# Kernel optimization log

Measured on AMD Instinct MI355X. Metric: run time of the kernel, lower is better.

The kernel has to match this reference:

```python
import jax, jax.numpy as jnp
import numpy as np

EPS = 1e-7  # K.epsilon()

def setup_inputs() -> dict:
    key = jax.random.key(0)
    k1, k2, k3 = jax.random.split(key, 3)
    B, T, D = 32, 2048, 512
    x = jax.random.normal(k1, (B, T, D), dtype=jnp.float32)
    W = jax.random.normal(k2, (D, D), dtype=jnp.float32) * (1.0 / np.sqrt(D))
    b = jnp.zeros((D,), dtype=jnp.float32)
    u = jax.random.normal(k3, (D,), dtype=jnp.float32) * (1.0 / np.sqrt(D))
    return {"x": x, "W": W, "b": b, "u": u}

def reference(x, W, b, u):
    # uit = tanh(x @ W + b)  -> [B, T, D]
    uit = jnp.tanh(jnp.einsum('btd,de->bte', x, W) + b)
    # scores: sum over feature dim of uit * u -> [B, T]
    ait = jnp.einsum('btd,d->bt', uit, u)
    # exp + normalize over T (no mask); matches original exp/sum form
    a = jnp.exp(ait)
    a = a / (jnp.sum(a, axis=1, keepdims=True) + EPS)
    # weighted sum pooling over T -> [B, D]
    return jnp.einsum('btd,bt->bd', x, a)
```

## Files before the change

kernel.cpp:

```cpp
#include <hip/hip_runtime.h>
#include <math.h>

#define D_DIM 512

typedef short short8v __attribute__((ext_vector_type(8)));
typedef unsigned short ushort8v __attribute__((ext_vector_type(8)));
typedef float f32x16 __attribute__((ext_vector_type(16)));

__device__ inline unsigned short f2bf(float f) {
    union { float f; unsigned int u; } a; a.f = f;
    unsigned int u = a.u;
    unsigned int r = (u + 0x7fffu + ((u >> 16) & 1u)) >> 16;
    return (unsigned short)r;
}

__global__ __launch_bounds__(256) void wt_kernel(const float* __restrict__ W,
                                                 unsigned short* __restrict__ Wb) {
    int g = blockIdx.x * 256 + threadIdx.x;
    int k = g >> 7;
    int e4 = (g & 127) * 4;
    float4 v = *(const float4*)(W + (size_t)k * D_DIM + e4);
    Wb[(size_t)(e4 + 0) * D_DIM + k] = f2bf(v.x);
    Wb[(size_t)(e4 + 1) * D_DIM + k] = f2bf(v.y);
    Wb[(size_t)(e4 + 2) * D_DIM + k] = f2bf(v.z);
    Wb[(size_t)(e4 + 3) * D_DIM + k] = f2bf(v.w);
}

constexpr int LDE = 40;

__global__ __launch_bounds__(256, 2) void gemm_ait_mfma(
    const float* __restrict__ x, const unsigned short* __restrict__ Wb,
    const float* __restrict__ bias, const float* __restrict__ u,
    float* __restrict__ ait)
{
    __shared__ __align__(16) unsigned short xs[64 * LDE];
    __shared__ __align__(16) unsigned short wsh[512 * LDE];
    __shared__ float rowpart[4][64];

    const int tid  = threadIdx.x;
    const int wave = tid >> 6;
    const int lane = tid & 63;
    const int half = lane >> 5;
    const int nl   = lane & 31;
    const int m0   = blockIdx.x * 64;

    f32x16 acc[2][4];
    #pragma unroll
    for (int mi = 0; mi < 2; ++mi)
        #pragma unroll
        for (int ni = 0; ni < 4; ++ni)
            #pragma unroll
            for (int r = 0; r < 16; ++r) acc[mi][ni][r] = 0.f;

    const int xr = tid >> 2;
    const int xc = tid & 3;

    for (int kk = 0; kk < D_DIM; kk += 32) {
        {
            const float* xp = x + (size_t)(m0 + xr) * D_DIM + kk + xc * 8;
            float4 a0 = *(const float4*)xp;
            float4 a1 = *(const float4*)(xp + 4);
            ushort8v pk;
            pk[0] = f2bf(a0.x); pk[1] = f2bf(a0.y); pk[2] = f2bf(a0.z); pk[3] = f2bf(a0.w);
            pk[4] = f2bf(a1.x); pk[5] = f2bf(a1.y); pk[6] = f2bf(a1.z); pk[7] = f2bf(a1.w);
            *(ushort8v*)&xs[xr * LDE + xc * 8] = pk;
        }
        #pragma unroll
        for (int p = 0; p < 8; ++p) {
            int chunk = tid + p * 256;
            int e  = chunk >> 2;
            int ci = chunk & 3;
            ushort8v wv = *(const ushort8v*)&Wb[(size_t)e * D_DIM + kk + ci * 8];
            *(ushort8v*)&wsh[e * LDE + ci * 8] = wv;
        }
        __syncthreads();

        #pragma unroll
        for (int ks = 0; ks < 2; ++ks) {
            short8v af[2], bfr[4];
            #pragma unroll
            for (int mi = 0; mi < 2; ++mi)
                af[mi] = *(const short8v*)&xs[(mi * 32 + nl) * LDE + ks * 16 + half * 8];
            #pragma unroll
            for (int ni = 0; ni < 4; ++ni)
                bfr[ni] = *(const short8v*)&wsh[(wave * 128 + ni * 32 + nl) * LDE + ks * 16 + half * 8];
            #pragma unroll
            for (int mi = 0; mi < 2; ++mi)
                #pragma unroll
                for (int ni = 0; ni < 4; ++ni)
                    acc[mi][ni] = __builtin_amdgcn_mfma_f32_32x32x16_bf16(
                        af[mi], bfr[ni], acc[mi][ni], 0, 0, 0);
        }
        __syncthreads();
    }

    float rowsum[2][16];
    #pragma unroll
    for (int mi = 0; mi < 2; ++mi)
        #pragma unroll
        for (int r = 0; r < 16; ++r) rowsum[mi][r] = 0.f;

    #pragma unroll
    for (int mi = 0; mi < 2; ++mi) {
        #pragma unroll
        for (int ni = 0; ni < 4; ++ni) {
            int col = wave * 128 + ni * 32 + nl;
            float be = bias[col], ue = u[col];
            #pragma unroll
            for (int r = 0; r < 16; ++r)
                rowsum[mi][r] += tanhf(acc[mi][ni][r] + be) * ue;
        }
    }
    #pragma unroll
    for (int mi = 0; mi < 2; ++mi)
        #pragma unroll
        for (int r = 0; r < 16; ++r) {
            float v = rowsum[mi][r];
            v += __shfl_xor(v, 1, 64);
            v += __shfl_xor(v, 2, 64);
            v += __shfl_xor(v, 4, 64);
            v += __shfl_xor(v, 8, 64);
            v += __shfl_xor(v, 16, 64);
            rowsum[mi][r] = v;
        }
    if (nl == 0) {
        #pragma unroll
        for (int mi = 0; mi < 2; ++mi)
            #pragma unroll
            for (int r = 0; r < 16; ++r) {
                int row = mi * 32 + (r & 3) + 8 * (r >> 2) + 4 * half;
                rowpart[wave][row] = rowsum[mi][r];
            }
    }
    __syncthreads();
    if (tid < 64)
        ait[m0 + tid] = rowpart[0][tid] + rowpart[1][tid] + rowpart[2][tid] + rowpart[3][tid];
}

__global__ __launch_bounds__(256) void gemm_ait_f32(
    const float* __restrict__ x, const float* __restrict__ W,
    const float* __restrict__ bias, const float* __restrict__ u,
    float* __restrict__ ait)
{
    __shared__ float xsf[64][68];
    __shared__ float wshf[64][132];
    const int tid = threadIdx.x;
    const int tx = tid & 15, ty = tid >> 4;
    const int m0 = blockIdx.x * 64;
    float rowsum[4] = {0.f, 0.f, 0.f, 0.f};
    for (int e0 = 0; e0 < D_DIM; e0 += 128) {
        float acc[4][8];
        #pragma unroll
        for (int i = 0; i < 4; ++i)
            #pragma unroll
            for (int j = 0; j < 8; ++j) acc[i][j] = 0.f;
        for (int kc = 0; kc < D_DIM; kc += 64) {
            #pragma unroll
            for (int i = 0; i < 4; ++i) {
                int idx = tid + i * 256;
                int r = idx >> 4, c = (idx & 15) * 4;
                *(float4*)&xsf[r][c] = *(const float4*)(x + (size_t)(m0 + r) * D_DIM + kc + c);
            }
            #pragma unroll
            for (int i = 0; i < 8; ++i) {
                int idx = tid + i * 256;
                int r = idx >> 5, c = (idx & 31) * 4;
                *(float4*)&wshf[r][c] = *(const float4*)(W + (size_t)(kc + r) * D_DIM + e0 + c);
            }
            __syncthreads();
            #pragma unroll 4
            for (int k = 0; k < 64; ++k) {
                float xv[4];
                #pragma unroll
                for (int i = 0; i < 4; ++i) xv[i] = xsf[ty * 4 + i][k];
                float4 w0 = *(const float4*)&wshf[k][tx * 8];
                float4 w1 = *(const float4*)&wshf[k][tx * 8 + 4];
                #pragma unroll
                for (int i = 0; i < 4; ++i) {
                    acc[i][0] += xv[i] * w0.x; acc[i][1] += xv[i] * w0.y;
                    acc[i][2] += xv[i] * w0.z; acc[i][3] += xv[i] * w0.w;
                    acc[i][4] += xv[i] * w1.x; acc[i][5] += xv[i] * w1.y;
                    acc[i][6] += xv[i] * w1.z; acc[i][7] += xv[i] * w1.w;
                }
            }
            __syncthreads();
        }
        #pragma unroll
        for (int j = 0; j < 8; ++j) {
            int e = e0 + tx * 8 + j;
            float be = bias[e], ue = u[e];
            #pragma unroll
            for (int i = 0; i < 4; ++i) rowsum[i] += tanhf(acc[i][j] + be) * ue;
        }
    }
    float* red = &xsf[0][0];
    #pragma unroll
    for (int i = 0; i < 4; ++i) red[(ty * 4 + i) * 16 + tx] = rowsum[i];
    __syncthreads();
    if (tid < 64) {
        float s = 0.f;
        #pragma unroll
        for (int j = 0; j < 16; ++j) s += red[tid * 16 + j];
        ait[m0 + tid] = s;
    }
}

__global__ __launch_bounds__(256) void softmax_kernel(float* __restrict__ ait, int T)
{
    const int b = blockIdx.x;
    float* p = ait + (size_t)b * T;
    const int tid = threadIdx.x;
    float ev[8];
    float local = 0.f;
    #pragma unroll
    for (int i = 0; i < 8; ++i) {
        ev[i] = expf(p[tid + i * 256]);
        local += ev[i];
    }
    #pragma unroll
    for (int off = 32; off > 0; off >>= 1)
        local += __shfl_down(local, off, 64);
    __shared__ float wsum[4];
    const int wv = tid >> 6, lane = tid & 63;
    if (lane == 0) wsum[wv] = local;
    __syncthreads();
    float total = wsum[0] + wsum[1] + wsum[2] + wsum[3];
    float inv = 1.0f / (total + 1e-7f);
    #pragma unroll
    for (int i = 0; i < 8; ++i) p[tid + i * 256] = ev[i] * inv;
}

__global__ __launch_bounds__(256) void pool_partial_kernel(
    const float* __restrict__ x, const float* __restrict__ a,
    float* __restrict__ partial, int T)
{
    const int chunks = T >> 8;
    const int b = blockIdx.x / chunks;
    const int c = blockIdx.x % chunks;
    const int tid = threadIdx.x;
    const int th = tid >> 7;
    const int d = (tid & 127) * 4;
    const int t0 = c * 256 + th * 128;

    const float* xp = x + ((size_t)b * T + t0) * D_DIM + d;
    const float* ap = a + (size_t)b * T + t0;

    float4 acc = {0.f, 0.f, 0.f, 0.f};
    for (int t = 0; t < 128; ++t) {
        float s = ap[t];
        float4 xv = *(const float4*)(xp + (size_t)t * D_DIM);
        acc.x += xv.x * s; acc.y += xv.y * s;
        acc.z += xv.z * s; acc.w += xv.w * s;
    }
    __shared__ float4 tmp[128];
    if (th == 1) tmp[tid & 127] = acc;
    __syncthreads();
    if (th == 0) {
        float4 o = tmp[tid];
        acc.x += o.x; acc.y += o.y; acc.z += o.z; acc.w += o.w;
        *(float4*)(partial + (size_t)blockIdx.x * D_DIM + d) = acc;
    }
}

__global__ __launch_bounds__(256) void pool_reduce_kernel(
    const float* __restrict__ partial, float* __restrict__ out, int chunks)
{
    const int b = blockIdx.x;
    const int tid = threadIdx.x;
    const int d = tid * 2;
    float2 acc = {0.f, 0.f};
    for (int c = 0; c < chunks; ++c) {
        float2 v = *(const float2*)(partial + ((size_t)b * chunks + c) * D_DIM + d);
        acc.x += v.x; acc.y += v.y;
    }
    *(float2*)(out + (size_t)b * D_DIM + d) = acc;
}

__global__ __launch_bounds__(256) void pool_atomic_kernel(
    const float* __restrict__ x, const float* __restrict__ a,
    float* __restrict__ out, int T)
{
    const int chunks = T >> 8;
    const int b = blockIdx.x / chunks;
    const int c = blockIdx.x % chunks;
    const int tid = threadIdx.x;
    const int d = tid * 2;
    const int t0 = c * 256;
    const float* xp = x + ((size_t)b * T + t0) * D_DIM + d;
    const float* ap = a + (size_t)b * T + t0;
    float2 acc = {0.f, 0.f};
    for (int t = 0; t < 256; ++t) {
        float s = ap[t];
        float2 xv = *(const float2*)(xp + (size_t)t * D_DIM);
        acc.x += xv.x * s; acc.y += xv.y * s;
    }
    float* o = out + (size_t)b * D_DIM + d;
    atomicAdd(o + 0, acc.x);
    atomicAdd(o + 1, acc.y);
}

extern "C" void kernel_launch(void* const* d_in, const int* in_sizes, int n_in,
                              void* d_out, int out_size, void* d_ws, size_t ws_size,
                              hipStream_t stream)
{
    const float* x    = (const float*)d_in[0];
    const float* W    = (const float*)d_in[1];
    const float* bias = (const float*)d_in[2];
    const float* u    = (const float*)d_in[3];
    float* out = (float*)d_out;

    const int Dd = in_sizes[2];
    const int M  = in_sizes[0] / Dd;
    const int B  = out_size / Dd;
    const int T  = M / B;
    const int chunks = T >> 8;

    const size_t wb_bytes   = (size_t)Dd * Dd * sizeof(unsigned short);
    const size_t ait_bytes  = (size_t)M * sizeof(float);
    const size_t part_bytes = (size_t)B * chunks * Dd * sizeof(float);

    if (ws_size >= wb_bytes + ait_bytes) {
        unsigned short* Wb = (unsigned short*)d_ws;
        float* ait = (float*)((char*)d_ws + wb_bytes);
        wt_kernel<<<dim3((Dd * Dd / 4) / 256), dim3(256), 0, stream>>>(W, Wb);
        gemm_ait_mfma<<<dim3(M / 64), dim3(256), 0, stream>>>(x, Wb, bias, u, ait);
        softmax_kernel<<<dim3(B), dim3(256), 0, stream>>>(ait, T);
        if (ws_size >= wb_bytes + ait_bytes + part_bytes) {
            float* partial = (float*)((char*)d_ws + wb_bytes + ait_bytes);
            pool_partial_kernel<<<dim3(B * chunks), dim3(256), 0, stream>>>(x, ait, partial, T);
            pool_reduce_kernel<<<dim3(B), dim3(256), 0, stream>>>(partial, out, chunks);
        } else {
            hipMemsetAsync(d_out, 0, (size_t)out_size * sizeof(float), stream);
            pool_atomic_kernel<<<dim3(B * chunks), dim3(256), 0, stream>>>(x, ait, out, T);
        }
    } else {
        float* ait = (float*)d_ws;
        gemm_ait_f32<<<dim3(M / 64), dim3(256), 0, stream>>>(x, W, bias, u, ait);
        softmax_kernel<<<dim3(B), dim3(256), 0, stream>>>(ait, T);
        hipMemsetAsync(d_out, 0, (size_t)out_size * sizeof(float), stream);
        pool_atomic_kernel<<<dim3(B * chunks), dim3(256), 0, stream>>>(x, ait, out, T);
    }
}
```

Measured before the change: 288.1 us.

## Prefetch next GEMM tile into registers, use fast tanh, split pooling finer

```diff
diff --git a/kernel.cpp b/kernel.cpp
--- a/kernel.cpp
+++ b/kernel.cpp
@@ -12,6 +12,11 @@
     unsigned int u = a.u;
     unsigned int r = (u + 0x7fffu + ((u >> 16) & 1u)) >> 16;
     return (unsigned short)r;
+}
+
+__device__ inline float fast_tanh(float y) {
+    float e2 = __expf(2.f * y);
+    return 1.f - __fdividef(2.f, e2 + 1.f);
 }
 
 __global__ __launch_bounds__(256) void wt_kernel(const float* __restrict__ W,
@@ -54,26 +59,44 @@
 
     const int xr = tid >> 2;
     const int xc = tid & 3;
+    const float* xbase = x + (size_t)(m0 + xr) * D_DIM + xc * 8;
+
+    int wg_off[8], wl_off[8];
+    #pragma unroll
+    for (int p = 0; p < 8; ++p) {
+        int chunk = tid + p * 256;
+        int e  = chunk >> 2;
+        int ci = chunk & 3;
+        wg_off[p] = e * D_DIM + ci * 8;
+        wl_off[p] = e * LDE + ci * 8;
+    }
+
+    float4 px0 = *(const float4*)(xbase);
+    float4 px1 = *(const float4*)(xbase + 4);
+    ushort8v pw[8];
+    #pragma unroll
+    for (int p = 0; p < 8; ++p)
+        pw[p] = *(const ushort8v*)&Wb[wg_off[p]];
 
     for (int kk = 0; kk < D_DIM; kk += 32) {
         {
-            const float* xp = x + (size_t)(m0 + xr) * D_DIM + kk + xc * 8;
-            float4 a0 = *(const float4*)xp;
-            float4 a1 = *(const float4*)(xp + 4);
             ushort8v pk;
-            pk[0] = f2bf(a0.x); pk[1] = f2bf(a0.y); pk[2] = f2bf(a0.z); pk[3] = f2bf(a0.w);
-            pk[4] = f2bf(a1.x); pk[5] = f2bf(a1.y); pk[6] = f2bf(a1.z); pk[7] = f2bf(a1.w);
+            pk[0] = f2bf(px0.x); pk[1] = f2bf(px0.y); pk[2] = f2bf(px0.z); pk[3] = f2bf(px0.w);
+            pk[4] = f2bf(px1.x); pk[5] = f2bf(px1.y); pk[6] = f2bf(px1.z); pk[7] = f2bf(px1.w);
             *(ushort8v*)&xs[xr * LDE + xc * 8] = pk;
         }
         #pragma unroll
-        for (int p = 0; p < 8; ++p) {
-            int chunk = tid + p * 256;
-            int e  = chunk >> 2;
-            int ci = chunk & 3;
-            ushort8v wv = *(const ushort8v*)&Wb[(size_t)e * D_DIM + kk + ci * 8];
-            *(ushort8v*)&wsh[e * LDE + ci * 8] = wv;
-        }
+        for (int p = 0; p < 8; ++p)
+            *(ushort8v*)&wsh[wl_off[p]] = pw[p];
         __syncthreads();
+
+        if (kk + 32 < D_DIM) {
+            px0 = *(const float4*)(xbase + kk + 32);
+            px1 = *(const float4*)(xbase + kk + 36);
+            #pragma unroll
+            for (int p = 0; p < 8; ++p)
+                pw[p] = *(const ushort8v*)&Wb[wg_off[p] + kk + 32];
+        }
 
         #pragma unroll
         for (int ks = 0; ks < 2; ++ks) {
@@ -108,7 +131,7 @@
             float be = bias[col], ue = u[col];
             #pragma unroll
             for (int r = 0; r < 16; ++r)
-                rowsum[mi][r] += tanhf(acc[mi][ni][r] + be) * ue;
+                rowsum[mi][r] += fast_tanh(acc[mi][ni][r] + be) * ue;
         }
     }
     #pragma unroll
@@ -234,19 +257,20 @@
     const float* __restrict__ x, const float* __restrict__ a,
     float* __restrict__ partial, int T)
 {
-    const int chunks = T >> 8;
+    const int chunks = T >> 7;
     const int b = blockIdx.x / chunks;
     const int c = blockIdx.x % chunks;
     const int tid = threadIdx.x;
     const int th = tid >> 7;
     const int d = (tid & 127) * 4;
-    const int t0 = c * 256 + th * 128;
+    const int t0 = c * 128;
 
     const float* xp = x + ((size_t)b * T + t0) * D_DIM + d;
     const float* ap = a + (size_t)b * T + t0;
 
     float4 acc = {0.f, 0.f, 0.f, 0.f};
-    for (int t = 0; t < 128; ++t) {
+    #pragma unroll 8
+    for (int t = th; t < 128; t += 2) {
         float s = ap[t];
         float4 xv = *(const float4*)(xp + (size_t)t * D_DIM);
         acc.x += xv.x * s; acc.y += xv.y * s;
@@ -313,7 +337,7 @@
     const int M  = in_sizes[0] / Dd;
     const int B  = out_size / Dd;
     const int T  = M / B;
-    const int chunks = T >> 8;
+    const int chunks = T >> 7;
 
     const size_t wb_bytes   = (size_t)Dd * Dd * sizeof(unsigned short);
     const size_t ait_bytes  = (size_t)M * sizeof(float);
@@ -331,13 +355,13 @@
             pool_reduce_kernel<<<dim3(B), dim3(256), 0, stream>>>(partial, out, chunks);
         } else {
             hipMemsetAsync(d_out, 0, (size_t)out_size * sizeof(float), stream);
-            pool_atomic_kernel<<<dim3(B * chunks), dim3(256), 0, stream>>>(x, ait, out, T);
+            pool_atomic_kernel<<<dim3(B * (T >> 8)), dim3(256), 0, stream>>>(x, ait, out, T);
         }
     } else {
         float* ait = (float*)d_ws;
         gemm_ait_f32<<<dim3(M / 64), dim3(256), 0, stream>>>(x, W, bias, u, ait);
         softmax_kernel<<<dim3(B), dim3(256), 0, stream>>>(ait, T);
         hipMemsetAsync(d_out, 0, (size_t)out_size * sizeof(float), stream);
-        pool_atomic_kernel<<<dim3(B * chunks), dim3(256), 0, stream>>>(x, ait, out, T);
-    }
-}
+        pool_atomic_kernel<<<dim3(B * (T >> 8)), dim3(256), 0, stream>>>(x, ait, out, T);
+    }
+}
```

Result: faster. 265.3 us (-7.9%).
